# Performance work log

Measured on AMD Instinct MI355X. Metric: run time of the kernel, lower is better.

Reference implementation:

```python
import jax, jax.numpy as jnp
import numpy as np
import math

NUM_HEADS = 16
FOCUS_FACTOR = 1.35  # 1.0 + congestion_level(0.3) + packet_loss(0.05)


def setup_inputs() -> dict:
    key = jax.random.key(0)
    ks = jax.random.split(key, 6)
    B, S, D = 2, 2048, 1024
    s = 1.0 / math.sqrt(D)
    return {
        "x": jax.random.normal(ks[0], (B, S, D), jnp.float32),
        "mask": jnp.ones((B, 1, S, S), jnp.int32),
        "Wq": jax.random.normal(ks[1], (D, D), jnp.float32) * s,
        "bq": jnp.zeros((D,), jnp.float32),
        "Wk": jax.random.normal(ks[2], (D, D), jnp.float32) * s,
        "bk": jnp.zeros((D,), jnp.float32),
        "Wv": jax.random.normal(ks[3], (D, D), jnp.float32) * s,
        "bv": jnp.zeros((D,), jnp.float32),
        "Wo": jax.random.normal(ks[4], (D, D), jnp.float32) * s,
        "bo": jnp.zeros((D,), jnp.float32),
    }


def reference(x, mask, Wq, bq, Wk, bk, Wv, bv, Wo, bo):
    B, S, D = x.shape
    H = NUM_HEADS
    hd = D // H
    # linear projections (torch Linear: x @ W^T + b), split heads -> [B,H,S,hd]
    q = (x @ Wq.T + bq).reshape(B, S, H, hd).transpose(0, 2, 1, 3)
    k = (x @ Wk.T + bk).reshape(B, S, H, hd).transpose(0, 2, 1, 3)
    v = (x @ Wv.T + bv).reshape(B, S, H, hd).transpose(0, 2, 1, 3)
    # rotary embedding in the source is an identity pass-through
    scores = jnp.einsum("bhqd,bhkd->bhqk", q, k) / math.sqrt(hd)
    scores = jnp.where(mask == 0, jnp.float32(-1e9), scores)
    scores = scores * jnp.float32(FOCUS_FACTOR)  # network focus factor
    attn = jax.nn.softmax(scores, axis=-1)  # dropout is identity in eval
    attended = jnp.einsum("bhqk,bhkd->bhqd", attn, v)
    attended = attended.transpose(0, 2, 1, 3).reshape(B, S, D)
    out = attended @ Wo.T + bo
    avg_attention = attn.mean(axis=1)  # [B, S, S]
    return out, avg_attention
```

## Files before the change

kernel.cpp:

```cpp
#include <hip/hip_runtime.h>
#include <cstdint>

typedef __bf16 bf16x8 __attribute__((ext_vector_type(8)));
typedef __bf16 bf16x4 __attribute__((ext_vector_type(4)));
typedef short  s16x8  __attribute__((ext_vector_type(8)));
typedef float  f32x4  __attribute__((ext_vector_type(4)));
typedef unsigned int uint32;
typedef uint32 u32x2 __attribute__((ext_vector_type(2)));
typedef unsigned long long u64;

#define SB 2048
#define DD 1024
#define HH 16
#define HDD 64
#define BB 2
#define C2LOG 0.2434547882f
#define NEGBIG2 (-1.9476383e9f)

__device__ __forceinline__ ushort f2bf(float f){
  uint32 u = __builtin_bit_cast(uint32, f);
  u += 0x7fffu + ((u >> 16) & 1u);
  return (ushort)(u >> 16);
}
__device__ __forceinline__ bf16x8 ldb128(const void* p){
  return __builtin_bit_cast(bf16x8, *(const s16x8*)p);
}
__device__ __forceinline__ void gl_lds16(const void* g, void* l){
  __builtin_amdgcn_global_load_lds((const __attribute__((address_space(1))) void*)g,
                                   (__attribute__((address_space(3))) void*)l, 16, 0, 0);
}
__device__ __forceinline__ float exp2r(float x){
  float r; asm("v_exp_f32 %0, %1" : "=v"(r) : "v"(x)); return r;
}

__global__ __launch_bounds__(256) void k_prep(
    const float* __restrict__ x, const int* __restrict__ mask,
    const float* __restrict__ Wq, const float* __restrict__ Wk,
    const float* __restrict__ Wv, const float* __restrict__ Wo,
    ushort* __restrict__ xb, u64* __restrict__ bits,
    ushort* __restrict__ wqb, ushort* __restrict__ wkb,
    ushort* __restrict__ wvb, ushort* __restrict__ wob)
{
  int bid = blockIdx.x;
  if (bid < 32768){
    int i = bid * 256 + threadIdx.x;
    u64 bm = __ballot(mask[i] != 0);
    if ((threadIdx.x & 63) == 0) bits[i >> 6] = bm;
  } else if (bid < 36864){
    int i = (bid - 32768) * 256 + threadIdx.x;
    float4 v = ((const float4*)x)[i];
    ushort4 o;
    o.x = f2bf(v.x); o.y = f2bf(v.y); o.z = f2bf(v.z); o.w = f2bf(v.w);
    ((ushort4*)xb)[i] = o;
  } else {
    int sub = bid - 36864;
    int zz = sub >> 10;
    const float* in = (zz == 0) ? Wq : (zz == 1) ? Wk : (zz == 2) ? Wv : Wo;
    ushort* out     = (zz == 0) ? wqb : (zz == 1) ? wkb : (zz == 2) ? wvb : wob;
    int i = (sub & 1023) * 256 + threadIdx.x;
    float4 v = ((const float4*)in)[i];
    ushort4 o;
    o.x = f2bf(v.x); o.y = f2bf(v.y); o.z = f2bf(v.z); o.w = f2bf(v.w);
    ((ushort4*)out)[i] = o;
  }
}

template<int MODE>
__device__ __forceinline__ void gemm_body(
    const ushort* __restrict__ A, const ushort* __restrict__ W,
    const float* __restrict__ bias, float scl,
    ushort* __restrict__ outp, float* __restrict__ outf,
    int rowBase, int colBase, ushort* lsA, ushort* lsB)
{
  const int t = threadIdx.x;
  const int l = t & 63, w = t >> 6;
  const int g16 = l >> 4, r16 = l & 15;
  const int wr = w >> 1, wc = w & 1;
  f32x4 zero = {0.f, 0.f, 0.f, 0.f};
  f32x4 acc[4][4];
  #pragma unroll
  for (int m = 0; m < 4; m++)
    #pragma unroll
    for (int n = 0; n < 4; n++) acc[m][n] = zero;

  auto stage = [&](int kt, int buf){
    #pragma unroll
    for (int i = 0; i < 2; i++){
      int c = t + i * 256;
      int row = c >> 2, cin = c & 3;
      int g = cin ^ ((row >> 1) & 3);
      gl_lds16(A + (size_t)(rowBase + row) * DD + kt * 32 + g * 8, (char*)lsA + buf * 8192 + c * 16);
      gl_lds16(W + (size_t)(colBase + row) * DD + kt * 32 + g * 8, (char*)lsB + buf * 8192 + c * 16);
    }
  };
  stage(0, 0);
  int cur = 0;
  for (int kt = 0; kt < 32; ++kt){
    __syncthreads();
    if (kt + 1 < 32) stage(kt + 1, cur ^ 1);
    bf16x8 af[4], bfr[4];
    #pragma unroll
    for (int m = 0; m < 4; m++){
      int row = wr * 64 + m * 16 + r16;
      af[m] = ldb128((char*)lsA + cur * 8192 + row * 64 + ((g16 ^ ((row >> 1) & 3)) << 4));
    }
    #pragma unroll
    for (int n = 0; n < 4; n++){
      int row = wc * 64 + n * 16 + r16;
      bfr[n] = ldb128((char*)lsB + cur * 8192 + row * 64 + ((g16 ^ ((row >> 1) & 3)) << 4));
    }
    #pragma unroll
    for (int m = 0; m < 4; m++)
      #pragma unroll
      for (int n = 0; n < 4; n++)
        acc[m][n] = __builtin_amdgcn_mfma_f32_16x16x32_bf16(af[m], bfr[n], acc[m][n], 0, 0, 0);
    cur ^= 1;
  }
  #pragma unroll
  for (int m = 0; m < 4; m++){
    #pragma unroll
    for (int n = 0; n < 4; n++){
      int ng = colBase + wc * 64 + n * 16 + r16;
      float bval = bias[ng];
      if (MODE == 2){
        int h = ng >> 6, d = ng & 63;
        int s0 = rowBase + wr * 64 + m * 16 + g16 * 4;
        int b = s0 >> 11, s = s0 & 2047;
        ushort4 o;
        o.x = f2bf((acc[m][n][0] + bval) * scl);
        o.y = f2bf((acc[m][n][1] + bval) * scl);
        o.z = f2bf((acc[m][n][2] + bval) * scl);
        o.w = f2bf((acc[m][n][3] + bval) * scl);
        *(ushort4*)(outp + ((size_t)(b * HH + h) * HDD + d) * SB + s) = o;
      } else {
        #pragma unroll
        for (int j = 0; j < 4; j++){
          int r = rowBase + wr * 64 + m * 16 + g16 * 4 + j;
          float v = (acc[m][n][j] + bval) * scl;
          if (MODE == 0){
            int h = ng >> 6, d = ng & 63;
            int b = r >> 11, s = r & 2047;
            outp[(((size_t)(b * HH + h) * SB + s) << 6) + d] = f2bf(v);
          } else {
            outf[(size_t)r * DD + ng] = v;
          }
        }
      }
    }
  }
}

__device__ __forceinline__ void xcd_patch(int& rowBase, int& colBase){
  int xcd = blockIdx.x, i = blockIdx.y;
  rowBase = ((xcd & 3) * 8 + (i & 7)) * 128;
  colBase = ((xcd >> 2) * 4 + (i >> 3)) * 128;
}

__global__ __launch_bounds__(256) void k_gemm_qkv(
    const ushort* __restrict__ A,
    const ushort* __restrict__ Wq, const ushort* __restrict__ Wk, const ushort* __restrict__ Wv,
    const float* __restrict__ bq, const float* __restrict__ bk, const float* __restrict__ bv,
    ushort* __restrict__ Q, ushort* __restrict__ K, ushort* __restrict__ Vt)
{
  __shared__ ushort lsA[2][4096];
  __shared__ ushort lsB[2][4096];
  int rowBase, colBase;
  xcd_patch(rowBase, colBase);
  int z = blockIdx.z;
  if (z == 0)      gemm_body<0>(A, Wq, bq, C2LOG, Q, nullptr, rowBase, colBase, &lsA[0][0], &lsB[0][0]);
  else if (z == 1) gemm_body<0>(A, Wk, bk, 1.0f, K, nullptr, rowBase, colBase, &lsA[0][0], &lsB[0][0]);
  else             gemm_body<2>(A, Wv, bv, 1.0f, Vt, nullptr, rowBase, colBase, &lsA[0][0], &lsB[0][0]);
}

__global__ __launch_bounds__(256) void k_gemm_out(
    const ushort* __restrict__ A, const ushort* __restrict__ Wo,
    const float* __restrict__ bo, float* __restrict__ out)
{
  __shared__ ushort lsA[2][4096];
  __shared__ ushort lsB[2][4096];
  int rowBase, colBase;
  xcd_patch(rowBase, colBase);
  gemm_body<1>(A, Wo, bo, 1.0f, nullptr, out, rowBase, colBase, &lsA[0][0], &lsB[0][0]);
}

__device__ __forceinline__ void stage_kv2(const ushort* __restrict__ Kp,
                                          const ushort* __restrict__ Vp,
                                          ushort* dK, ushort* dV, int t){
  #pragma unroll
  for (int i = 0; i < 2; ++i){
    int c = t + 512 * i;
    int r = c >> 3, g = (c & 7) ^ (r & 7);
    gl_lds16(Kp + (size_t)r * HDD + g * 8, (char*)dK + c * 16);
  }
  #pragma unroll
  for (int i = 0; i < 2; ++i){
    int c = t + 512 * i;
    int r = c >> 4, cc = c & 15;
    int g = ((cc & 7) ^ (r & 7)) | (cc & 8);
    gl_lds16(Vp + (size_t)r * SB + g * 8, (char*)dV + c * 16);
  }
}

__global__ __launch_bounds__(512) void k_flash(
    const ushort* __restrict__ Q, const ushort* __restrict__ K, const ushort* __restrict__ Vt,
    const u64* __restrict__ mbits,
    ushort* __restrict__ att, float* __restrict__ ilarr)
{
  __shared__ ushort lsK[2][8192];
  __shared__ ushort lsV[2][10240];
  __shared__ ushort lsP[8][2048];
  const int t = threadIdx.x;
  const int l = t & 63, w = t >> 6;
  const int g16 = l >> 4, r16 = l & 15;
  const int bid = blockIdx.x;
  const int qt = (bid >> 3) & 7;
  const int hb = (bid >> 6) * 8 + (bid & 7);
  const int h = hb & 15, b = hb >> 4;
  const size_t ho = ((size_t)(b * HH + h)) * SB * HDD;
  const int qa = qt * 256 + w * 32 + r16;
  const int qb = qa + 16;

  bf16x8 aqa[2], aqb[2];
  #pragma unroll
  for (int ks = 0; ks < 2; ++ks){
    aqa[ks] = ldb128(Q + ho + (size_t)qa * HDD + ks * 32 + g16 * 8);
    aqb[ks] = ldb128(Q + ho + (size_t)qb * HDD + ks * 32 + g16 * 8);
  }
  const u64* mpa = mbits + ((size_t)b * SB + qa) * 32;
  const u64* mpb = mbits + ((size_t)b * SB + qb) * 32;

  f32x4 zero = {0.f, 0.f, 0.f, 0.f};
  f32x4 accA[4], accB[4], accLA = zero, accLB = zero;
  #pragma unroll
  for (int c = 0; c < 4; c++){ accA[c] = zero; accB[c] = zero; }

  if (t < 256) lsV[t >> 7][8192 + (t & 127)] = 0x3F80;

  const ushort* Kb = K + ho;
  const ushort* Vb = Vt + ho;
  stage_kv2(Kb, Vb, &lsK[0][0], &lsV[0][0], t);

  int cur = 0;
  for (int kk = 0; kk < 16; ++kk){
    __syncthreads();
    if (kk + 1 < 16)
      stage_kv2(Kb + (size_t)(kk + 1) * 128 * HDD, Vb + (size_t)(kk + 1) * 128,
                &lsK[cur ^ 1][0], &lsV[cur ^ 1][0], t);

    #pragma unroll
    for (int h2 = 0; h2 < 2; ++h2){
      const char* lk = (const char*)&lsK[cur][0] + h2 * 8192;
      const char* lv = (const char*)&lsV[cur][0] + h2 * 128;
      char* lp = (char*)&lsP[w][0];

      f32x4 za[4], zb[4];
      __builtin_amdgcn_s_setprio(1);
      #pragma unroll
      for (int f = 0; f < 4; ++f){
        za[f] = zero; zb[f] = zero;
        int row = 16 * f + r16;
        #pragma unroll
        for (int ks = 0; ks < 2; ++ks){
          bf16x8 kf = ldb128(lk + row * 128 + ((((ks << 2) + g16) ^ (row & 7)) << 4));
          za[f] = __builtin_amdgcn_mfma_f32_16x16x32_bf16(kf, aqa[ks], za[f], 0, 0, 0);
          zb[f] = __builtin_amdgcn_mfma_f32_16x16x32_bf16(kf, aqb[ks], zb[f], 0, 0, 0);
        }
      }
      __builtin_amdgcn_s_setprio(0);

      u64 mwa = mpa[2 * kk + h2], mwb = mpb[2 * kk + h2];
      float pa[4][4], pb[4][4];
      if (__all((mwa & mwb) == ~0ull)){
        #pragma unroll
        for (int f = 0; f < 4; ++f)
          #pragma unroll
          for (int j = 0; j < 4; ++j){
            pa[f][j] = exp2r(za[f][j]);
            pb[f][j] = exp2r(zb[f][j]);
          }
      } else {
        #pragma unroll
        for (int f = 0; f < 4; ++f)
          #pragma unroll
          for (int j = 0; j < 4; ++j){
            int bit = 16 * f + 4 * g16 + j;
            pa[f][j] = exp2r(((mwa >> bit) & 1ull) ? za[f][j] : NEGBIG2);
            pb[f][j] = exp2r(((mwb >> bit) & 1ull) ? zb[f][j] : NEGBIG2);
          }
      }

      {
        int wba = r16 * 128 + ((g16 & 1) << 3);
        int wbb = (r16 + 16) * 128 + ((g16 & 1) << 3);
        #pragma unroll
        for (int f = 0; f < 4; ++f){
          bf16x4 va_ = { (__bf16)pa[f][0], (__bf16)pa[f][1], (__bf16)pa[f][2], (__bf16)pa[f][3] };
          bf16x4 vb_ = { (__bf16)pb[f][0], (__bf16)pb[f][1], (__bf16)pb[f][2], (__bf16)pb[f][3] };
          int sw = ((2 * f + (g16 >> 1)) ^ (r16 & 7)) << 4;
          *(u32x2*)(lp + wba + sw) = __builtin_bit_cast(u32x2, va_);
          *(u32x2*)(lp + wbb + sw) = __builtin_bit_cast(u32x2, vb_);
        }
      }
      bf16x8 pfA[2], pfB[2];
      #pragma unroll
      for (int ks = 0; ks < 2; ++ks){
        int sw = (((ks << 2) + g16) ^ (r16 & 7)) << 4;
        pfA[ks] = ldb128(lp + r16 * 128 + sw);
        pfB[ks] = ldb128(lp + (r16 + 16) * 128 + sw);
      }

      __builtin_amdgcn_s_setprio(1);
      #pragma unroll
      for (int c = 0; c < 4; ++c){
        int row = 16 * c + r16;
        #pragma unroll
        for (int ks = 0; ks < 2; ++ks){
          bf16x8 vf = ldb128(lv + row * 256 + ((((ks << 2) + g16) ^ (row & 7)) << 4));
          accA[c] = __builtin_amdgcn_mfma_f32_16x16x32_bf16(vf, pfA[ks], accA[c], 0, 0, 0);
          accB[c] = __builtin_amdgcn_mfma_f32_16x16x32_bf16(vf, pfB[ks], accB[c], 0, 0, 0);
        }
      }
      {
        int row = 64 + r16;
        #pragma unroll
        for (int ks = 0; ks < 2; ++ks){
          bf16x8 of = ldb128(lv + row * 256 + ((((ks << 2) + g16) ^ (row & 7)) << 4));
          accLA = __builtin_amdgcn_mfma_f32_16x16x32_bf16(of, pfA[ks], accLA, 0, 0, 0);
          accLB = __builtin_amdgcn_mfma_f32_16x16x32_bf16(of, pfB[ks], accLB, 0, 0, 0);
        }
      }
      __builtin_amdgcn_s_setprio(0);
    }
    cur ^= 1;
  }

  float ila = 1.0f / __shfl(accLA[0], r16);
  float ilb = 1.0f / __shfl(accLB[0], r16);
  #pragma unroll
  for (int c = 0; c < 4; ++c){
    ushort4 oa, ob;
    oa.x = f2bf(accA[c][0] * ila); oa.y = f2bf(accA[c][1] * ila);
    oa.z = f2bf(accA[c][2] * ila); oa.w = f2bf(accA[c][3] * ila);
    ob.x = f2bf(accB[c][0] * ilb); ob.y = f2bf(accB[c][1] * ilb);
    ob.z = f2bf(accB[c][2] * ilb); ob.w = f2bf(accB[c][3] * ilb);
    *(ushort4*)(att + ((size_t)b * SB + qa) * DD + h * HDD + c * 16 + 4 * g16) = oa;
    *(ushort4*)(att + ((size_t)b * SB + qb) * DD + h * HDD + c * 16 + 4 * g16) = ob;
  }
  if (g16 == 0){
    ilarr[(size_t)(b * HH + h) * SB + qa] = ila;
    ilarr[(size_t)(b * HH + h) * SB + qb] = ilb;
  }
}

__global__ __launch_bounds__(512) void k_avg(
    const ushort* __restrict__ Q, const ushort* __restrict__ K,
    const u64* __restrict__ mbits,
    const float* __restrict__ ilarr, float* __restrict__ avg)
{
  __shared__ ushort lsQ[2][8192];
  __shared__ ushort lsK[2][8192];
  const int t = threadIdx.x;
  const int l = t & 63, w = t >> 6;
  const int g16 = l >> 4, r16 = l & 15;
  const int b = blockIdx.z, qt = blockIdx.y, kt = blockIdx.x;
  const int qbase = qt * 128, kbase = kt * 128;
  const int qr0 = qbase + w * 16 + g16 * 4;

  u64 mw[4][2];
  #pragma unroll
  for (int j = 0; j < 4; j++){
    mw[j][0] = mbits[((size_t)b * SB + qr0 + j) * 32 + 2 * kt];
    mw[j][1] = mbits[((size_t)b * SB + qr0 + j) * 32 + 2 * kt + 1];
  }
  bool fast = __all((mw[0][0] & mw[0][1] & mw[1][0] & mw[1][1] &
                     mw[2][0] & mw[2][1] & mw[3][0] & mw[3][1]) == ~0ull);

  f32x4 zero = {0.f, 0.f, 0.f, 0.f};
  f32x4 acc[8];
  #pragma unroll
  for (int f = 0; f < 8; f++) acc[f] = zero;

  const size_t hstep = (size_t)SB * HDD;
  const ushort* Qp = Q + (size_t)b * HH * hstep + (size_t)qbase * HDD;
  const ushort* Kp = K + (size_t)b * HH * hstep + (size_t)kbase * HDD;

  for (int hh = 0; hh < 8; ++hh){
    __syncthreads();
    #pragma unroll
    for (int p = 0; p < 2; ++p){
      int h = 2 * hh + p;
      #pragma unroll
      for (int i = 0; i < 2; ++i){
        int c = t + i * 512;
        int r = c >> 3, g = (c & 7) ^ (r & 7);
        gl_lds16(Qp + (size_t)h * hstep + (size_t)r * HDD + g * 8, (char*)&lsQ[p][0] + c * 16);
        gl_lds16(Kp + (size_t)h * hstep + (size_t)r * HDD + g * 8, (char*)&lsK[p][0] + c * 16);
      }
    }
    __syncthreads();

    #pragma unroll
    for (int p = 0; p < 2; ++p){
      int h = 2 * hh + p;
      int qrow = w * 16 + r16;
      bf16x8 a0 = ldb128((char*)&lsQ[p][0] + qrow * 128 + (((0 + g16) ^ (qrow & 7)) << 4));
      bf16x8 a1 = ldb128((char*)&lsQ[p][0] + qrow * 128 + (((4 + g16) ^ (qrow & 7)) << 4));
      float ilh[4];
      #pragma unroll
      for (int j = 0; j < 4; j++)
        ilh[j] = ilarr[(size_t)(b * HH + h) * SB + qr0 + j];

      #pragma unroll
      for (int f = 0; f < 8; ++f){
        int row = 16 * f + r16;
        bf16x8 b0 = ldb128((char*)&lsK[p][0] + row * 128 + (((0 + g16) ^ (row & 7)) << 4));
        bf16x8 b1 = ldb128((char*)&lsK[p][0] + row * 128 + (((4 + g16) ^ (row & 7)) << 4));
        f32x4 z = zero;
        z = __builtin_amdgcn_mfma_f32_16x16x32_bf16(a0, b0, z, 0, 0, 0);
        z = __builtin_amdgcn_mfma_f32_16x16x32_bf16(a1, b1, z, 0, 0, 0);
        if (fast){
          #pragma unroll
          for (int j = 0; j < 4; j++)
            acc[f][j] += exp2r(z[j]) * ilh[j];
        } else {
          int kl = 16 * f + r16;
          int word = kl >> 6, bit = kl & 63;
          #pragma unroll
          for (int j = 0; j < 4; j++){
            float s = ((mw[j][word] >> bit) & 1ull) ? z[j] : NEGBIG2;
            acc[f][j] += exp2r(s) * ilh[j];
          }
        }
      }
    }
  }
  #pragma unroll
  for (int f = 0; f < 8; f++)
    #pragma unroll
    for (int j = 0; j < 4; j++){
      int qr = qr0 + j;
      int kc = kbase + 16 * f + r16;
      avg[((size_t)b * SB + qr) * SB + kc] = acc[f][j] * 0.0625f;
    }
}

extern "C" void kernel_launch(void* const* d_in, const int* in_sizes, int n_in,
                              void* d_out, int out_size, void* d_ws, size_t ws_size,
                              hipStream_t stream)
{
  const float* x  = (const float*)d_in[0];
  const int* mask = (const int*)d_in[1];
  const float* Wq = (const float*)d_in[2];
  const float* bq = (const float*)d_in[3];
  const float* Wk = (const float*)d_in[4];
  const float* bk = (const float*)d_in[5];
  const float* Wv = (const float*)d_in[6];
  const float* bv = (const float*)d_in[7];
  const float* Wo = (const float*)d_in[8];
  const float* bo = (const float*)d_in[9];
  float* out = (float*)d_out;
  float* avg = out + (size_t)BB * SB * DD;

  char* ws = (char*)d_ws;
  ushort* xb   = (ushort*)(ws);
  ushort* wqb  = (ushort*)(ws + (8ull  << 20));
  ushort* wkb  = (ushort*)(ws + (10ull << 20));
  ushort* wvb  = (ushort*)(ws + (12ull << 20));
  ushort* wob  = (ushort*)(ws + (14ull << 20));
  ushort* Qb   = (ushort*)(ws + (16ull << 20));
  ushort* Kb   = (ushort*)(ws + (24ull << 20));
  ushort* Vtb  = (ushort*)(ws + (32ull << 20));
  ushort* att  = (ushort*)(ws + (40ull << 20));
  float*  ilarr= (float*) (ws + (48ull << 20));
  u64*    mbits= (u64*)   (ws + (49ull << 20));

  k_prep<<<40960, 256, 0, stream>>>(x, mask, Wq, Wk, Wv, Wo,
                                    xb, mbits, wqb, wkb, wvb, wob);
  k_gemm_qkv<<<dim3(8, 32, 3), 256, 0, stream>>>(xb, wqb, wkb, wvb,
                                                 bq, bk, bv, Qb, Kb, Vtb);
  k_flash<<<256, 512, 0, stream>>>(Qb, Kb, Vtb, mbits, att, ilarr);
  k_avg<<<dim3(16, 16, 2), 512, 0, stream>>>(Qb, Kb, mbits, ilarr, avg);
  k_gemm_out<<<dim3(8, 32, 1), 256, 0, stream>>>(att, wob, bo, out);
}
```

Baseline: 173.2 us.

## Merge output projection GEMM and attention-average kernel into one launch

The output projection GEMM and the averaged-attention kernel are now one launch of 768 blocks. The first 256 blocks run the GEMM on half their threads, while the other half spin on matching __syncthreads calls. The remaining 512 blocks compute the averaged attention. The two independent stages can then overlap on the GPU and one launch is saved, but the GEMM blocks now occupy 512-thread slots with half their threads idle, and correctness depends on the barrier count matching gemm_body's internal syncs.

```diff
diff --git a/kernel.cpp b/kernel.cpp
--- a/kernel.cpp
+++ b/kernel.cpp
@@ -150,8 +150,8 @@
   }
 }
 
-__device__ __forceinline__ void xcd_patch(int& rowBase, int& colBase){
-  int xcd = blockIdx.x, i = blockIdx.y;
+__device__ __forceinline__ void xcd_patch2(int bid, int& rowBase, int& colBase){
+  int xcd = bid & 7, i = bid >> 3;
   rowBase = ((xcd & 3) * 8 + (i & 7)) * 128;
   colBase = ((xcd >> 2) * 4 + (i >> 3)) * 128;
 }
@@ -165,22 +165,11 @@
   __shared__ ushort lsA[2][4096];
   __shared__ ushort lsB[2][4096];
   int rowBase, colBase;
-  xcd_patch(rowBase, colBase);
+  xcd_patch2(blockIdx.x + blockIdx.y * 8, rowBase, colBase);
   int z = blockIdx.z;
   if (z == 0)      gemm_body<0>(A, Wq, bq, C2LOG, Q, nullptr, rowBase, colBase, &lsA[0][0], &lsB[0][0]);
   else if (z == 1) gemm_body<0>(A, Wk, bk, 1.0f, K, nullptr, rowBase, colBase, &lsA[0][0], &lsB[0][0]);
   else             gemm_body<2>(A, Wv, bv, 1.0f, Vt, nullptr, rowBase, colBase, &lsA[0][0], &lsB[0][0]);
-}
-
-__global__ __launch_bounds__(256) void k_gemm_out(
-    const ushort* __restrict__ A, const ushort* __restrict__ Wo,
-    const float* __restrict__ bo, float* __restrict__ out)
-{
-  __shared__ ushort lsA[2][4096];
-  __shared__ ushort lsB[2][4096];
-  int rowBase, colBase;
-  xcd_patch(rowBase, colBase);
-  gemm_body<1>(A, Wo, bo, 1.0f, nullptr, out, rowBase, colBase, &lsA[0][0], &lsB[0][0]);
 }
 
 __device__ __forceinline__ void stage_kv2(const ushort* __restrict__ Kp,
@@ -352,17 +341,36 @@
   }
 }
 
-__global__ __launch_bounds__(512) void k_avg(
+__global__ __launch_bounds__(512) void k_avg_out(
+    const ushort* __restrict__ att, const ushort* __restrict__ wob,
+    const float* __restrict__ bo, float* __restrict__ out,
     const ushort* __restrict__ Q, const ushort* __restrict__ K,
     const u64* __restrict__ mbits,
     const float* __restrict__ ilarr, float* __restrict__ avg)
 {
-  __shared__ ushort lsQ[2][8192];
-  __shared__ ushort lsK[2][8192];
+  __shared__ ushort smem[32768];
+  const int bid = blockIdx.x;
   const int t = threadIdx.x;
+
+  if (bid < 256){
+    int rowBase, colBase;
+    xcd_patch2(bid, rowBase, colBase);
+    if (t < 256){
+      gemm_body<1>(att, wob, bo, 1.0f, nullptr, out, rowBase, colBase,
+                   smem, smem + 8192);
+    } else {
+      #pragma unroll 1
+      for (int k = 0; k < 32; ++k) __syncthreads();
+    }
+    return;
+  }
+
+  const int bid2 = bid - 256;
+  const int kt = bid2 & 15, qt = (bid2 >> 4) & 15, b = bid2 >> 8;
+  ushort* lsQ0 = smem;
+  ushort* lsK0 = smem + 16384;
   const int l = t & 63, w = t >> 6;
   const int g16 = l >> 4, r16 = l & 15;
-  const int b = blockIdx.z, qt = blockIdx.y, kt = blockIdx.x;
   const int qbase = qt * 128, kbase = kt * 128;
   const int qr0 = qbase + w * 16 + g16 * 4;
 
@@ -393,8 +401,8 @@
       for (int i = 0; i < 2; ++i){
         int c = t + i * 512;
         int r = c >> 3, g = (c & 7) ^ (r & 7);
-        gl_lds16(Qp + (size_t)h * hstep + (size_t)r * HDD + g * 8, (char*)&lsQ[p][0] + c * 16);
-        gl_lds16(Kp + (size_t)h * hstep + (size_t)r * HDD + g * 8, (char*)&lsK[p][0] + c * 16);
+        gl_lds16(Qp + (size_t)h * hstep + (size_t)r * HDD + g * 8, (char*)(lsQ0 + p * 8192) + c * 16);
+        gl_lds16(Kp + (size_t)h * hstep + (size_t)r * HDD + g * 8, (char*)(lsK0 + p * 8192) + c * 16);
       }
     }
     __syncthreads();
@@ -403,8 +411,8 @@
     for (int p = 0; p < 2; ++p){
       int h = 2 * hh + p;
       int qrow = w * 16 + r16;
-      bf16x8 a0 = ldb128((char*)&lsQ[p][0] + qrow * 128 + (((0 + g16) ^ (qrow & 7)) << 4));
-      bf16x8 a1 = ldb128((char*)&lsQ[p][0] + qrow * 128 + (((4 + g16) ^ (qrow & 7)) << 4));
+      bf16x8 a0 = ldb128((char*)(lsQ0 + p * 8192) + qrow * 128 + (((0 + g16) ^ (qrow & 7)) << 4));
+      bf16x8 a1 = ldb128((char*)(lsQ0 + p * 8192) + qrow * 128 + (((4 + g16) ^ (qrow & 7)) << 4));
       float ilh[4];
       #pragma unroll
       for (int j = 0; j < 4; j++)
@@ -413,8 +421,8 @@
       #pragma unroll
       for (int f = 0; f < 8; ++f){
         int row = 16 * f + r16;
-        bf16x8 b0 = ldb128((char*)&lsK[p][0] + row * 128 + (((0 + g16) ^ (row & 7)) << 4));
-        bf16x8 b1 = ldb128((char*)&lsK[p][0] + row * 128 + (((4 + g16) ^ (row & 7)) << 4));
+        bf16x8 b0 = ldb128((char*)(lsK0 + p * 8192) + row * 128 + (((0 + g16) ^ (row & 7)) << 4));
+        bf16x8 b1 = ldb128((char*)(lsK0 + p * 8192) + row * 128 + (((4 + g16) ^ (row & 7)) << 4));
         f32x4 z = zero;
         z = __builtin_amdgcn_mfma_f32_16x16x32_bf16(a0, b0, z, 0, 0, 0);
         z = __builtin_amdgcn_mfma_f32_16x16x32_bf16(a1, b1, z, 0, 0, 0);
@@ -479,6 +487,5 @@
   k_gemm_qkv<<<dim3(8, 32, 3), 256, 0, stream>>>(xb, wqb, wkb, wvb,
                                                  bq, bk, bv, Qb, Kb, Vtb);
   k_flash<<<256, 512, 0, stream>>>(Qb, Kb, Vtb, mbits, att, ilarr);
-  k_avg<<<dim3(16, 16, 2), 512, 0, stream>>>(Qb, Kb, mbits, ilarr, avg);
-  k_gemm_out<<<dim3(8, 32, 1), 256, 0, stream>>>(att, wob, bo, out);
-}
+  k_avg_out<<<768, 512, 0, stream>>>(att, wob, bo, out, Qb, Kb, mbits, ilarr, avg);
+}
```

Result: faster. 160.4 us (-7.4%).
